# Kernel tuning notes

Measured on AMD Instinct MI355X. Metric: run time of the kernel, lower is better.

Reference implementation:

```python
import math
import jax, jax.numpy as jnp
import numpy as np

B, T = 65536, 34
VOCAB, TOK_DIM, POS_DIM, D_MODEL, FFN_DIM, HEAD_DIM = 14, 2, 3, 5, 2, 5
EPS = 1e-5

def _pos_flat_idx():
    # replicate _build_pos_map: 10 digits, Z_HI, 10 digits, Z_HI, 10 digits, special0, special1
    sources, indices = [], []
    for _ in range(3):
        for i in range(10):
            sources.append(0); indices.append(i)
        sources.append(2); indices.append(len([s for s in sources if s == 2]) - 1)
    # fix: the torch code appends (2,0),(2,1) after first two digit blocks and (1,0),(2,2) after the third
    sources, indices = [], []
    for i in range(10): sources.append(0); indices.append(i)
    sources.append(2); indices.append(0)
    for i in range(10): sources.append(0); indices.append(i)
    sources.append(2); indices.append(1)
    for i in range(10): sources.append(0); indices.append(i)
    sources.append(1); indices.append(0)
    sources.append(2); indices.append(2)
    src = np.array(sources); idx = np.array(indices)
    # table layout: rows 0..9 digit_pos, row 10 z_hi_pos, rows 11..13 special (learned0, learned1, eos)
    offs = np.array([0, 10, 11])
    return offs[src] + idx  # (34,)

POS_FLAT = jnp.asarray(_pos_flat_idx())
CAUSAL = jnp.tril(jnp.ones((T, T), dtype=bool))

def _rms(x, w):
    return x * jax.lax.rsqrt(jnp.mean(x * x, -1, keepdims=True) + EPS) * w

def setup_inputs():
    key = jax.random.key(0)
    ks = jax.random.split(key, 16)
    n = lambda i, shape: jax.random.normal(ks[i], shape, jnp.float32) * 0.5
    return {
        'idx': jax.random.randint(ks[0], (B, T), 0, VOCAB),
        'tok_emb': n(1, (VOCAB, TOK_DIM)),
        'spiral_amp': jnp.float32(1.0),
        'spiral_phase': jnp.float32(0.1),
        'spiral_slope': jnp.float32(1.0 / 9.0),
        'spiral_offset': jnp.float32(0.05),
        'pos_corr_slope': jnp.float32(0.01),
        'pos_corr_intercept': jnp.float32(0.02),
        'z_hi_pos': n(2, (1, POS_DIM)),
        'special_pos': n(3, (2, POS_DIM)),
        'q_w': n(4, (HEAD_DIM, POS_DIM)),
        'v_w': n(5, (HEAD_DIM, TOK_DIM)),
        'out_A': n(6, (HEAD_DIM, 2)),
        'out_B': n(7, (2, D_MODEL)),
        'q_phase': n(8, (1,)),
        'ln1_w': jnp.ones((D_MODEL,), jnp.float32),
        'ln2_w': jnp.ones((D_MODEL,), jnp.float32),
        'lnf_w': jnp.ones((D_MODEL,), jnp.float32),
        'fc1_w': n(9, (FFN_DIM, D_MODEL)),
        'fc1_b': n(10, (FFN_DIM,)),
        'fc2_w': n(11, (D_MODEL, FFN_DIM)),
        'fc2_b': n(12, (D_MODEL,)),
        'head_w': n(13, (TOK_DIM, D_MODEL)),
    }

def reference(idx, tok_emb, spiral_amp, spiral_phase, spiral_slope, spiral_offset,
              pos_corr_slope, pos_corr_intercept, z_hi_pos, special_pos,
              q_w, v_w, out_A, out_B, q_phase, ln1_w, ln2_w, lnf_w,
              fc1_w, fc1_b, fc2_w, fc2_b, head_w):
    # learned spiral digit positions (10, 3)
    i = jnp.arange(10, dtype=jnp.float32)
    angle = 2.0 * math.pi * i / 10.0 + spiral_phase
    base = jnp.stack([spiral_amp * jnp.cos(angle),
                      spiral_amp * jnp.sin(angle),
                      spiral_slope * i + spiral_offset], -1)
    corr = pos_corr_intercept + pos_corr_slope * i
    digit_pos = base * (1.0 + corr)[:, None]
    table = jnp.concatenate([digit_pos, z_hi_pos, special_pos,
                             jnp.zeros((1, POS_DIM), jnp.float32)], 0)  # (14, 3)
    pos = table[POS_FLAT]  # (T, 3)

    tok = tok_emb[idx]  # (B, T, 2)
    x = jnp.concatenate([tok, jnp.broadcast_to(pos, (idx.shape[0], T, POS_DIM))], -1)  # (B,T,5)

    h = _rms(x, ln1_w)
    q = jnp.einsum('btp,dp->btd', h[..., TOK_DIM:], q_w)  # (B,T,5)
    k = q  # q_proj applied to same input for both q and k
    v = jnp.einsum('btp,dp->btd', h[..., :TOK_DIM], v_w)  # (B,T,5)

    # per-head 2D rotation on first 4 dims (HEAD_DIM//2 = 2 pairs), dim 4 unchanged
    c, s = jnp.cos(q_phase[0]), jnp.sin(q_phase[0])
    q0, q1 = q[..., 0:4:2], q[..., 1:4:2]
    q_rot = jnp.concatenate([
        jnp.stack([q0 * c - q1 * s, q0 * s + q1 * c], -1).reshape(q.shape[:-1] + (4,)),
        q[..., 4:]], -1)

    att = jnp.einsum('btd,bsd->bts', q_rot, k) / math.sqrt(HEAD_DIM)
    att = jnp.where(CAUSAL, att, -jnp.inf)
    att = jax.nn.softmax(att, -1)
    out = jnp.einsum('bts,bsd->btd', att, v)  # (B,T,5)

    x = x + (out @ out_A) @ out_B  # low-rank out_proj
    hh = _rms(x, ln2_w)
    x = x + (jax.nn.gelu(hh @ fc1_w.T + fc1_b, approximate=False) @ fc2_w.T + fc2_b)
    x = _rms(x, lnf_w)
    return (x @ head_w.T) @ tok_emb.T  # (B, T, 14)
```

## Files before the change

### kernel.cpp

```cpp
#include <hip/hip_runtime.h>
#include <math.h>

#define T_SEQ 34
#define NTOK 14
#define NE (T_SEQ * NTOK)

__global__ __launch_bounds__(256) void micro_fused_kernel(
    const int* __restrict__ idx,
    const float* __restrict__ tok_emb,
    const float* __restrict__ s_amp, const float* __restrict__ s_phase,
    const float* __restrict__ s_slope, const float* __restrict__ s_offset,
    const float* __restrict__ pc_slope, const float* __restrict__ pc_int,
    const float* __restrict__ z_hi, const float* __restrict__ spec,
    const float* __restrict__ q_w, const float* __restrict__ v_w,
    const float* __restrict__ out_A, const float* __restrict__ out_B,
    const float* __restrict__ q_phase,
    const float* __restrict__ ln1_w, const float* __restrict__ ln2_w,
    const float* __restrict__ lnf_w,
    const float* __restrict__ fc1_w, const float* __restrict__ fc1_b,
    const float* __restrict__ fc2_w, const float* __restrict__ fc2_b,
    const float* __restrict__ head_w,
    float* __restrict__ out, int N)
{
    __shared__ float H8[NE * 8];
    __shared__ float C3[NE * 4];
    __shared__ float PosT[T_SEQ * 3];
    __shared__ float TE[NTOK * 2];
    __shared__ float PMs[10];
    __shared__ float Ws[5 * NTOK];
    __shared__ float ln2s[5], lnfs[5], fc1ws[10], fc1bs[2], fc2ws[10], fc2bs[5];
    __shared__ int toks[9 * T_SEQ];

    const int tid = threadIdx.x;

    {
        const float amp = s_amp[0], ph = s_phase[0], slp = s_slope[0], off = s_offset[0];
        const float pcs = pc_slope[0], pci = pc_int[0];
        const float cph = cosf(q_phase[0]), sph = sinf(q_phase[0]);
        const float invs5 = 0.44721359549995793f;
        for (int e = tid; e < NE; e += 256) {
            int t = e / NTOK, tk = e - t * NTOK;
            float px, py, pz;
            if (t == 33)      { px = 0.f;     py = 0.f;     pz = 0.f; }
            else if (t == 32) { px = z_hi[0]; py = z_hi[1]; pz = z_hi[2]; }
            else if (t == 10) { px = spec[0]; py = spec[1]; pz = spec[2]; }
            else if (t == 21) { px = spec[3]; py = spec[4]; pz = spec[5]; }
            else {
                int i = (t < 10) ? t : (t < 21 ? t - 11 : t - 22);
                float fi = (float)i;
                float ang = 0.62831853071795864769f * fi + ph;
                float mlt = 1.f + pci + pcs * fi;
                px = amp * cosf(ang) * mlt;
                py = amp * sinf(ang) * mlt;
                pz = (slp * fi + off) * mlt;
            }
            if (tk == 0) { PosT[t*3] = px; PosT[t*3+1] = py; PosT[t*3+2] = pz; }
            float x0 = tok_emb[tk * 2], x1 = tok_emb[tk * 2 + 1];
            float ssum = x0*x0 + x1*x1 + px*px + py*py + pz*pz;
            float r = rsqrtf(ssum * 0.2f + 1e-5f);
            float h0 = x0 * r * ln1_w[0], h1 = x1 * r * ln1_w[1];
            float h2 = px * r * ln1_w[2], h3 = py * r * ln1_w[3], h4 = pz * r * ln1_w[4];
            float q0 = q_w[0]  * h2 + q_w[1]  * h3 + q_w[2]  * h4;
            float q1 = q_w[3]  * h2 + q_w[4]  * h3 + q_w[5]  * h4;
            float q2 = q_w[6]  * h2 + q_w[7]  * h3 + q_w[8]  * h4;
            float q3 = q_w[9]  * h2 + q_w[10] * h3 + q_w[11] * h4;
            float q4 = q_w[12] * h2 + q_w[13] * h3 + q_w[14] * h4;
            float r0 = q0 * cph - q1 * sph, r1 = q0 * sph + q1 * cph;
            float r2c = q2 * cph - q3 * sph, r3 = q2 * sph + q3 * cph;
            float c0 = (r0*q_w[0] + r1*q_w[3] + r2c*q_w[6] + r3*q_w[9]  + q4*q_w[12]) * invs5;
            float c1 = (r0*q_w[1] + r1*q_w[4] + r2c*q_w[7] + r3*q_w[10] + q4*q_w[13]) * invs5;
            float c2 = (r0*q_w[2] + r1*q_w[5] + r2c*q_w[8] + r3*q_w[11] + q4*q_w[14]) * invs5;
            float* H = &H8[e * 8];
            H[0] = h2; H[1] = h3; H[2] = h4; H[3] = h0; H[4] = h1;
            float* C = &C3[e * 4];
            C[0] = c0; C[1] = c1; C[2] = c2; C[3] = 0.f;
        }
    }
    if (tid < 28) TE[tid] = tok_emb[tid];
    if (tid < 70) {
        int d = tid / NTOK, v = tid - d * NTOK;
        Ws[tid] = head_w[d] * tok_emb[v * 2] + head_w[5 + d] * tok_emb[v * 2 + 1];
    }
    if (tid < 10) {
        int j = tid >> 1, c = tid & 1;
        float acc = 0.f;
        for (int i = 0; i < 5; ++i) {
            float m5 = out_A[i*2] * out_B[j] + out_A[i*2+1] * out_B[5 + j];
            acc += m5 * v_w[i*2 + c];
        }
        PMs[tid] = acc;
    }
    if (tid < 5)  { ln2s[tid] = ln2_w[tid]; lnfs[tid] = lnf_w[tid]; fc2bs[tid] = fc2_b[tid]; }
    if (tid < 10) { fc1ws[tid] = fc1_w[tid]; fc2ws[tid] = fc2_w[tid]; }
    if (tid < 2)  { fc1bs[tid] = fc1_b[tid]; }

    const int blockStart = blockIdx.x * 256;
    const int b0 = blockStart / T_SEQ;
    int lastLin = blockStart + 255; if (lastLin >= N) lastLin = N - 1;
    const int nrows = lastLin / T_SEQ - b0 + 1;
    for (int i = tid; i < nrows * T_SEQ; i += 256)
        toks[i] = idx[b0 * T_SEQ + i];

    __syncthreads();

    const int lin = blockStart + tid;
    if (lin >= N) return;
    const int b = lin / T_SEQ;
    const int t = lin - b * T_SEQ;
    const int rowBase = (b - b0) * T_SEQ;

    const int tokt = toks[rowBase + t];
    const float4 c3 = *(const float4*)&C3[(t * NTOK + tokt) * 4];
    const float xv0 = TE[tokt * 2], xv1 = TE[tokt * 2 + 1];
    const float xv2 = PosT[t*3], xv3 = PosT[t*3+1], xv4 = PosT[t*3+2];

    float l = 0.f, a0 = 0.f, a1 = 0.f;
    for (int s = 0; s <= t; ++s) {
        int o = (s * NTOK + toks[rowBase + s]) * 8;
        float4 h = *(const float4*)&H8[o];
        float h1 = H8[o + 4];
        float sc = fmaf(c3.x, h.x, fmaf(c3.y, h.y, c3.z * h.z));
        float p = __expf(sc);
        l += p;
        a0 = fmaf(p, h.w, a0);
        a1 = fmaf(p, h1, a1);
    }
    const float il = 1.f / l;
    a0 *= il; a1 *= il;

    float y[5];
#pragma unroll
    for (int j = 0; j < 5; ++j)
        y[j] = (j == 0 ? xv0 : j == 1 ? xv1 : j == 2 ? xv2 : j == 3 ? xv3 : xv4)
             + PMs[j*2] * a0 + PMs[j*2+1] * a1;

    float s2 = y[0]*y[0] + y[1]*y[1] + y[2]*y[2] + y[3]*y[3] + y[4]*y[4];
    float r2 = rsqrtf(s2 * 0.2f + 1e-5f);
    float hh[5];
#pragma unroll
    for (int j = 0; j < 5; ++j) hh[j] = y[j] * r2 * ln2s[j];

    float u0 = fc1bs[0], u1 = fc1bs[1];
#pragma unroll
    for (int j = 0; j < 5; ++j) { u0 += hh[j] * fc1ws[j]; u1 += hh[j] * fc1ws[5 + j]; }
    float g0 = 0.5f * u0 * (1.f + erff(u0 * 0.70710678118654752f));
    float g1 = 0.5f * u1 * (1.f + erff(u1 * 0.70710678118654752f));

    float y2[5]; float s3 = 0.f;
#pragma unroll
    for (int j = 0; j < 5; ++j) {
        y2[j] = y[j] + g0 * fc2ws[j * 2] + g1 * fc2ws[j * 2 + 1] + fc2bs[j];
        s3 += y2[j] * y2[j];
    }
    float r3 = rsqrtf(s3 * 0.2f + 1e-5f);
    float z[5];
#pragma unroll
    for (int j = 0; j < 5; ++j) z[j] = y2[j] * r3 * lnfs[j];

    float res[14];
#pragma unroll
    for (int v = 0; v < 14; ++v)
        res[v] = z[0] * Ws[v] + z[1] * Ws[14 + v] + z[2] * Ws[28 + v]
               + z[3] * Ws[42 + v] + z[4] * Ws[56 + v];

    float2* op = (float2*)(out + (size_t)lin * 14);
#pragma unroll
    for (int v = 0; v < 7; ++v) op[v] = make_float2(res[2 * v], res[2 * v + 1]);
}

extern "C" void kernel_launch(void* const* d_in, const int* in_sizes, int n_in,
                              void* d_out, int out_size, void* d_ws, size_t ws_size,
                              hipStream_t stream) {
    const int N = in_sizes[0];
    const int grid = (N + 255) / 256;
    micro_fused_kernel<<<grid, 256, 0, stream>>>(
        (const int*)d_in[0],
        (const float*)d_in[1], (const float*)d_in[2], (const float*)d_in[3],
        (const float*)d_in[4], (const float*)d_in[5], (const float*)d_in[6],
        (const float*)d_in[7], (const float*)d_in[8], (const float*)d_in[9],
        (const float*)d_in[10], (const float*)d_in[11], (const float*)d_in[12],
        (const float*)d_in[13], (const float*)d_in[14], (const float*)d_in[15],
        (const float*)d_in[16], (const float*)d_in[17], (const float*)d_in[18],
        (const float*)d_in[19], (const float*)d_in[20], (const float*)d_in[21],
        (const float*)d_in[22],
        (float*)d_out, N);
}
```

Before: 230.3 us.

## Process 32 sequences per block with gathered per-row key tables and staged attention

Each 512-thread block now handles 32 full sequences. Per-position key data is gathered into a [s][row] shared table so the causal loop walks strided, conflict-free entries instead of re-indexing tokens on every step. The fixed per-block setup (table build, weight loads) is spread over more work, exp is replaced by exp2f with log2e folded into the query scale, and attention is split into three phases: gather, attention, then MLP and output. This adds two extra barriers, more shared memory per block and an uneven attention loop across threads, which may lower occupancy.

```diff
diff --git a/kernel.cpp b/kernel.cpp
--- a/kernel.cpp
+++ b/kernel.cpp
@@ -4,8 +4,11 @@
 #define T_SEQ 34
 #define NTOK 14
 #define NE (T_SEQ * NTOK)
-
-__global__ __launch_bounds__(256) void micro_fused_kernel(
+#define ROWS 32
+#define BLK 512
+#define RP1 (ROWS + 1)
+
+__global__ __launch_bounds__(BLK) void micro_fused_kernel(
     const int* __restrict__ idx,
     const float* __restrict__ tok_emb,
     const float* __restrict__ s_amp, const float* __restrict__ s_phase,
@@ -22,59 +25,68 @@
     const float* __restrict__ head_w,
     float* __restrict__ out, int N)
 {
-    __shared__ float H8[NE * 8];
-    __shared__ float C3[NE * 4];
+    __shared__ float4 H4[NE];
+    __shared__ float  H1f[NE];
+    __shared__ float4 C3[NE];
+    __shared__ float4 Gm[T_SEQ * ROWS];
+    __shared__ float  G1[T_SEQ * ROWS];
+    __shared__ float2 Av[T_SEQ * RP1];
+    __shared__ int    toks[ROWS * T_SEQ];
     __shared__ float PosT[T_SEQ * 3];
     __shared__ float TE[NTOK * 2];
     __shared__ float PMs[10];
     __shared__ float Ws[5 * NTOK];
     __shared__ float ln2s[5], lnfs[5], fc1ws[10], fc1bs[2], fc2ws[10], fc2bs[5];
-    __shared__ int toks[9 * T_SEQ];
 
     const int tid = threadIdx.x;
-
-    {
+    const int b0 = blockIdx.x * ROWS;
+    const int elemBase = b0 * T_SEQ;
+
+    for (int i = tid; i < ROWS * T_SEQ; i += BLK) {
+        int g = elemBase + i;
+        toks[i] = (g < N) ? idx[g] : 0;
+    }
+
+    if (tid < NE) {
         const float amp = s_amp[0], ph = s_phase[0], slp = s_slope[0], off = s_offset[0];
         const float pcs = pc_slope[0], pci = pc_int[0];
         const float cph = cosf(q_phase[0]), sph = sinf(q_phase[0]);
-        const float invs5 = 0.44721359549995793f;
-        for (int e = tid; e < NE; e += 256) {
-            int t = e / NTOK, tk = e - t * NTOK;
-            float px, py, pz;
-            if (t == 33)      { px = 0.f;     py = 0.f;     pz = 0.f; }
-            else if (t == 32) { px = z_hi[0]; py = z_hi[1]; pz = z_hi[2]; }
-            else if (t == 10) { px = spec[0]; py = spec[1]; pz = spec[2]; }
-            else if (t == 21) { px = spec[3]; py = spec[4]; pz = spec[5]; }
-            else {
-                int i = (t < 10) ? t : (t < 21 ? t - 11 : t - 22);
-                float fi = (float)i;
-                float ang = 0.62831853071795864769f * fi + ph;
-                float mlt = 1.f + pci + pcs * fi;
-                px = amp * cosf(ang) * mlt;
-                py = amp * sinf(ang) * mlt;
-                pz = (slp * fi + off) * mlt;
-            }
-            if (tk == 0) { PosT[t*3] = px; PosT[t*3+1] = py; PosT[t*3+2] = pz; }
-            float x0 = tok_emb[tk * 2], x1 = tok_emb[tk * 2 + 1];
-            float ssum = x0*x0 + x1*x1 + px*px + py*py + pz*pz;
-            float r = rsqrtf(ssum * 0.2f + 1e-5f);
-            float h0 = x0 * r * ln1_w[0], h1 = x1 * r * ln1_w[1];
-            float h2 = px * r * ln1_w[2], h3 = py * r * ln1_w[3], h4 = pz * r * ln1_w[4];
-            float q0 = q_w[0]  * h2 + q_w[1]  * h3 + q_w[2]  * h4;
-            float q1 = q_w[3]  * h2 + q_w[4]  * h3 + q_w[5]  * h4;
-            float q2 = q_w[6]  * h2 + q_w[7]  * h3 + q_w[8]  * h4;
-            float q3 = q_w[9]  * h2 + q_w[10] * h3 + q_w[11] * h4;
-            float q4 = q_w[12] * h2 + q_w[13] * h3 + q_w[14] * h4;
-            float r0 = q0 * cph - q1 * sph, r1 = q0 * sph + q1 * cph;
-            float r2c = q2 * cph - q3 * sph, r3 = q2 * sph + q3 * cph;
-            float c0 = (r0*q_w[0] + r1*q_w[3] + r2c*q_w[6] + r3*q_w[9]  + q4*q_w[12]) * invs5;
-            float c1 = (r0*q_w[1] + r1*q_w[4] + r2c*q_w[7] + r3*q_w[10] + q4*q_w[13]) * invs5;
-            float c2 = (r0*q_w[2] + r1*q_w[5] + r2c*q_w[8] + r3*q_w[11] + q4*q_w[14]) * invs5;
-            float* H = &H8[e * 8];
-            H[0] = h2; H[1] = h3; H[2] = h4; H[3] = h0; H[4] = h1;
-            float* C = &C3[e * 4];
-            C[0] = c0; C[1] = c1; C[2] = c2; C[3] = 0.f;
-        }
+        const float cscale = 0.44721359549995793f * 1.4426950408889634f;
+        const int e = tid;
+        const int t = e / NTOK, tk = e - t * NTOK;
+        float px, py, pz;
+        if (t == 33)      { px = 0.f;     py = 0.f;     pz = 0.f; }
+        else if (t == 32) { px = z_hi[0]; py = z_hi[1]; pz = z_hi[2]; }
+        else if (t == 10) { px = spec[0]; py = spec[1]; pz = spec[2]; }
+        else if (t == 21) { px = spec[3]; py = spec[4]; pz = spec[5]; }
+        else {
+            int i = (t < 10) ? t : (t < 21 ? t - 11 : t - 22);
+            float fi = (float)i;
+            float ang = 0.62831853071795864769f * fi + ph;
+            float mlt = 1.f + pci + pcs * fi;
+            px = amp * cosf(ang) * mlt;
+            py = amp * sinf(ang) * mlt;
+            pz = (slp * fi + off) * mlt;
+        }
+        if (tk == 0) { PosT[t*3] = px; PosT[t*3+1] = py; PosT[t*3+2] = pz; }
+        float x0 = tok_emb[tk * 2], x1 = tok_emb[tk * 2 + 1];
+        float ssum = x0*x0 + x1*x1 + px*px + py*py + pz*pz;
+        float rn = rsqrtf(ssum * 0.2f + 1e-5f);
+        float h0 = x0 * rn * ln1_w[0], h1 = x1 * rn * ln1_w[1];
+        float h2 = px * rn * ln1_w[2], h3 = py * rn * ln1_w[3], h4 = pz * rn * ln1_w[4];
+        float q0 = q_w[0]  * h2 + q_w[1]  * h3 + q_w[2]  * h4;
+        float q1 = q_w[3]  * h2 + q_w[4]  * h3 + q_w[5]  * h4;
+        float q2 = q_w[6]  * h2 + q_w[7]  * h3 + q_w[8]  * h4;
+        float q3 = q_w[9]  * h2 + q_w[10] * h3 + q_w[11] * h4;
+        float q4 = q_w[12] * h2 + q_w[13] * h3 + q_w[14] * h4;
+        float r0 = q0 * cph - q1 * sph, r1 = q0 * sph + q1 * cph;
+        float r2c = q2 * cph - q3 * sph, r3 = q2 * sph + q3 * cph;
+        float c0 = (r0*q_w[0] + r1*q_w[3] + r2c*q_w[6] + r3*q_w[9]  + q4*q_w[12]) * cscale;
+        float c1 = (r0*q_w[1] + r1*q_w[4] + r2c*q_w[7] + r3*q_w[10] + q4*q_w[13]) * cscale;
+        float c2 = (r0*q_w[2] + r1*q_w[5] + r2c*q_w[8] + r3*q_w[11] + q4*q_w[14]) * cscale;
+        H4[e] = make_float4(h2, h3, h4, h0);
+        H1f[e] = h1;
+        C3[e] = make_float4(c0, c1, c2, 0.f);
     }
     if (tid < 28) TE[tid] = tok_emb[tid];
     if (tid < 70) {
@@ -94,86 +106,98 @@
     if (tid < 10) { fc1ws[tid] = fc1_w[tid]; fc2ws[tid] = fc2_w[tid]; }
     if (tid < 2)  { fc1bs[tid] = fc1_b[tid]; }
 
-    const int blockStart = blockIdx.x * 256;
-    const int b0 = blockStart / T_SEQ;
-    int lastLin = blockStart + 255; if (lastLin >= N) lastLin = N - 1;
-    const int nrows = lastLin / T_SEQ - b0 + 1;
-    for (int i = tid; i < nrows * T_SEQ; i += 256)
-        toks[i] = idx[b0 * T_SEQ + i];
-
     __syncthreads();
 
-    const int lin = blockStart + tid;
-    if (lin >= N) return;
-    const int b = lin / T_SEQ;
-    const int t = lin - b * T_SEQ;
-    const int rowBase = (b - b0) * T_SEQ;
-
-    const int tokt = toks[rowBase + t];
-    const float4 c3 = *(const float4*)&C3[(t * NTOK + tokt) * 4];
-    const float xv0 = TE[tokt * 2], xv1 = TE[tokt * 2 + 1];
-    const float xv2 = PosT[t*3], xv3 = PosT[t*3+1], xv4 = PosT[t*3+2];
-
-    float l = 0.f, a0 = 0.f, a1 = 0.f;
-    for (int s = 0; s <= t; ++s) {
-        int o = (s * NTOK + toks[rowBase + s]) * 8;
-        float4 h = *(const float4*)&H8[o];
-        float h1 = H8[o + 4];
-        float sc = fmaf(c3.x, h.x, fmaf(c3.y, h.y, c3.z * h.z));
-        float p = __expf(sc);
-        l += p;
-        a0 = fmaf(p, h.w, a0);
-        a1 = fmaf(p, h1, a1);
-    }
-    const float il = 1.f / l;
-    a0 *= il; a1 *= il;
-
-    float y[5];
-#pragma unroll
-    for (int j = 0; j < 5; ++j)
-        y[j] = (j == 0 ? xv0 : j == 1 ? xv1 : j == 2 ? xv2 : j == 3 ? xv3 : xv4)
-             + PMs[j*2] * a0 + PMs[j*2+1] * a1;
-
-    float s2 = y[0]*y[0] + y[1]*y[1] + y[2]*y[2] + y[3]*y[3] + y[4]*y[4];
-    float r2 = rsqrtf(s2 * 0.2f + 1e-5f);
-    float hh[5];
-#pragma unroll
-    for (int j = 0; j < 5; ++j) hh[j] = y[j] * r2 * ln2s[j];
-
-    float u0 = fc1bs[0], u1 = fc1bs[1];
-#pragma unroll
-    for (int j = 0; j < 5; ++j) { u0 += hh[j] * fc1ws[j]; u1 += hh[j] * fc1ws[5 + j]; }
-    float g0 = 0.5f * u0 * (1.f + erff(u0 * 0.70710678118654752f));
-    float g1 = 0.5f * u1 * (1.f + erff(u1 * 0.70710678118654752f));
-
-    float y2[5]; float s3 = 0.f;
-#pragma unroll
-    for (int j = 0; j < 5; ++j) {
-        y2[j] = y[j] + g0 * fc2ws[j * 2] + g1 * fc2ws[j * 2 + 1] + fc2bs[j];
-        s3 += y2[j] * y2[j];
-    }
-    float r3 = rsqrtf(s3 * 0.2f + 1e-5f);
-    float z[5];
-#pragma unroll
-    for (int j = 0; j < 5; ++j) z[j] = y2[j] * r3 * lnfs[j];
-
-    float res[14];
-#pragma unroll
-    for (int v = 0; v < 14; ++v)
-        res[v] = z[0] * Ws[v] + z[1] * Ws[14 + v] + z[2] * Ws[28 + v]
-               + z[3] * Ws[42 + v] + z[4] * Ws[56 + v];
-
-    float2* op = (float2*)(out + (size_t)lin * 14);
-#pragma unroll
-    for (int v = 0; v < 7; ++v) op[v] = make_float2(res[2 * v], res[2 * v + 1]);
+    for (int i = tid; i < T_SEQ * ROWS; i += BLK) {
+        int s = i >> 5;
+        int r = i & (ROWS - 1);
+        int tok = toks[r * T_SEQ + s];
+        int e = s * NTOK + tok;
+        Gm[i] = H4[e];
+        G1[i] = H1f[e];
+    }
+    __syncthreads();
+
+    for (int ii = tid; ii < T_SEQ * ROWS; ii += BLK) {
+        int t = ii >> 5;
+        int r = ii & (ROWS - 1);
+        int tok = toks[r * T_SEQ + t];
+        float4 c3 = C3[t * NTOK + tok];
+        float l = 0.f, a0 = 0.f, a1 = 0.f;
+        const float4* gm = &Gm[r];
+        const float*  g1 = &G1[r];
+#pragma unroll 4
+        for (int s = 0; s <= t; ++s) {
+            float4 h  = gm[s * ROWS];
+            float h1v = g1[s * ROWS];
+            float sc = fmaf(c3.x, h.x, fmaf(c3.y, h.y, c3.z * h.z));
+            float p = exp2f(sc);
+            l += p;
+            a0 = fmaf(p, h.w, a0);
+            a1 = fmaf(p, h1v, a1);
+        }
+        float il = 1.f / l;
+        Av[t * RP1 + r] = make_float2(a0 * il, a1 * il);
+    }
+    __syncthreads();
+
+    for (int e2 = tid; e2 < ROWS * T_SEQ; e2 += BLK) {
+        int lin = elemBase + e2;
+        if (lin >= N) break;
+        int r = e2 / T_SEQ;
+        int t = e2 - r * T_SEQ;
+        int tok = toks[e2];
+        float2 a = Av[t * RP1 + r];
+        float xv0 = TE[tok * 2], xv1 = TE[tok * 2 + 1];
+        float xv2 = PosT[t*3], xv3 = PosT[t*3+1], xv4 = PosT[t*3+2];
+
+        float y[5];
+#pragma unroll
+        for (int j = 0; j < 5; ++j)
+            y[j] = (j == 0 ? xv0 : j == 1 ? xv1 : j == 2 ? xv2 : j == 3 ? xv3 : xv4)
+                 + PMs[j*2] * a.x + PMs[j*2+1] * a.y;
+
+        float s2 = y[0]*y[0] + y[1]*y[1] + y[2]*y[2] + y[3]*y[3] + y[4]*y[4];
+        float r2 = rsqrtf(s2 * 0.2f + 1e-5f);
+        float hh[5];
+#pragma unroll
+        for (int j = 0; j < 5; ++j) hh[j] = y[j] * r2 * ln2s[j];
+
+        float u0 = fc1bs[0], u1 = fc1bs[1];
+#pragma unroll
+        for (int j = 0; j < 5; ++j) { u0 += hh[j] * fc1ws[j]; u1 += hh[j] * fc1ws[5 + j]; }
+        float g0 = 0.5f * u0 * (1.f + erff(u0 * 0.70710678118654752f));
+        float g1v = 0.5f * u1 * (1.f + erff(u1 * 0.70710678118654752f));
+
+        float y2[5]; float s3 = 0.f;
+#pragma unroll
+        for (int j = 0; j < 5; ++j) {
+            y2[j] = y[j] + g0 * fc2ws[j * 2] + g1v * fc2ws[j * 2 + 1] + fc2bs[j];
+            s3 += y2[j] * y2[j];
+        }
+        float r3 = rsqrtf(s3 * 0.2f + 1e-5f);
+        float z[5];
+#pragma unroll
+        for (int j = 0; j < 5; ++j) z[j] = y2[j] * r3 * lnfs[j];
+
+        float res[14];
+#pragma unroll
+        for (int v = 0; v < 14; ++v)
+            res[v] = z[0] * Ws[v] + z[1] * Ws[14 + v] + z[2] * Ws[28 + v]
+                   + z[3] * Ws[42 + v] + z[4] * Ws[56 + v];
+
+        float2* op = (float2*)(out + (size_t)lin * 14);
+#pragma unroll
+        for (int v = 0; v < 7; ++v) op[v] = make_float2(res[2 * v], res[2 * v + 1]);
+    }
 }
 
 extern "C" void kernel_launch(void* const* d_in, const int* in_sizes, int n_in,
                               void* d_out, int out_size, void* d_ws, size_t ws_size,
                               hipStream_t stream) {
     const int N = in_sizes[0];
-    const int grid = (N + 255) / 256;
-    micro_fused_kernel<<<grid, 256, 0, stream>>>(
+    const int grid = (N + ROWS * T_SEQ - 1) / (ROWS * T_SEQ);
+    micro_fused_kernel<<<grid, BLK, 0, stream>>>(
         (const int*)d_in[0],
         (const float*)d_in[1], (const float*)d_in[2], (const float*)d_in[3],
         (const float*)d_in[4], (const float*)d_in[5], (const float*)d_in[6],
```

Result: slower. 248.2 us (+7.8%).
